# Performance work log

Hardware: AMD Instinct MI355X
Metric: run time of the kernel (lower is better)

The kernel has to match this reference:

```python
import jax, jax.numpy as jnp
import numpy as np

B, S, D, H = 1, 4096, 768, 12
HD = D // H  # 64

def setup_inputs() -> dict:
    key = jax.random.key(0)
    k1, k2, k3 = jax.random.split(key, 3)
    x = jax.random.normal(k1, (B, S, D), dtype=jnp.float32)
    W_attn = jax.random.normal(k2, (D, 3 * D), dtype=jnp.float32) * 0.02
    b_attn = jnp.zeros((3 * D,), dtype=jnp.float32)
    W_proj = jax.random.normal(k3, (D, D), dtype=jnp.float32) * 0.02
    b_proj = jnp.zeros((D,), dtype=jnp.float32)
    return {"x": x, "W_attn": W_attn, "b_attn": b_attn, "W_proj": W_proj, "b_proj": b_proj}

def reference(x, W_attn, b_attn, W_proj, b_proj):
    # qkv projection (Conv1D = x @ W + b)
    qkv = x @ W_attn + b_attn  # [B,S,3D]
    q, k, v = jnp.split(qkv, 3, axis=-1)
    def split_heads(t):
        return t.reshape(B, S, H, HD).transpose(0, 2, 1, 3)  # [B,H,S,HD]
    q, k, v = split_heads(q), split_heads(k), split_heads(v)
    # NOTE: original applies no 1/sqrt(head_dim) scaling
    scores = jnp.einsum('bhqd,bhkd->bhqk', q, k)  # [B,H,S,S]
    causal = jnp.tril(jnp.ones((S, S), dtype=bool))
    mask_value = jnp.finfo(scores.dtype).min
    scores = jnp.where(causal, scores, mask_value)
    attn = jax.nn.softmax(scores, axis=-1)
    # dropout is identity in eval mode
    out = jnp.einsum('bhqk,bhkd->bhqd', attn, v)  # [B,H,S,HD]
    out = out.transpose(0, 2, 1, 3).reshape(B, S, D)
    return out @ W_proj + b_proj
```

## Files before the change

kernel.cpp:

```cpp
#include <hip/hip_runtime.h>


typedef short bf16x8 __attribute__((ext_vector_type(8)));
typedef float f32x4 __attribute__((ext_vector_type(4)));
typedef unsigned short u16x8_t __attribute__((ext_vector_type(8)));
typedef unsigned short u16x4_t __attribute__((ext_vector_type(4)));

#define ATT_S  4096
#define ATT_D  768
#define ATT_3D 2304
#define ATT_H  12
#define LOG2E  1.44269504089f

__device__ __forceinline__ unsigned short f2b(float f) {
  union { float f; unsigned int u; } v; v.f = f;
  unsigned int r = v.u + 0x7fffu + ((v.u >> 16) & 1u);
  return (unsigned short)(r >> 16);
}

__device__ __forceinline__ f32x4 mfma16(bf16x8 a, bf16x8 b, f32x4 c) {
  return __builtin_amdgcn_mfma_f32_16x16x32_bf16(a, b, c, 0, 0, 0);
}

__device__ __forceinline__ void glds16(const void* g, void* l) {
  __builtin_amdgcn_global_load_lds((__attribute__((address_space(1))) void*)g,
                                   (__attribute__((address_space(3))) void*)l,
                                   16, 0, 0);
}

__device__ __forceinline__ int swz8(int row, int c) {
  return row * 64 + ((c ^ (row & 7)) << 3);
}


__global__ __launch_bounds__(256) void convert_f32_bf16(
    const float* __restrict__ in, unsigned short* __restrict__ out, int n4) {
  int i = blockIdx.x * 256 + threadIdx.x;
  if (i >= n4) return;
  float4 v = ((const float4*)in)[i];
  u16x4_t o;
  o[0] = f2b(v.x); o[1] = f2b(v.y); o[2] = f2b(v.z); o[3] = f2b(v.w);
  ((u16x4_t*)out)[i] = o;
}

__global__ __launch_bounds__(256) void transpose_conv(
    const float* __restrict__ W, unsigned short* __restrict__ WT, int K, int N) {
  __shared__ float tile[32][33];
  int bx = blockIdx.x, by = blockIdx.y;
  int tx = threadIdx.x & 31, ty = threadIdx.x >> 5;
#pragma unroll
  for (int k = 0; k < 4; k++)
    tile[ty + k * 8][tx] = W[(size_t)(by * 32 + ty + k * 8) * N + bx * 32 + tx];
  __syncthreads();
#pragma unroll
  for (int k = 0; k < 4; k++)
    WT[(size_t)(bx * 32 + ty + k * 8) * K + by * 32 + tx] = f2b(tile[tx][ty + k * 8]);
}


template <int BF16_OUT>
__global__ __launch_bounds__(256) void gemm_bias(
    const unsigned short* __restrict__ A, const unsigned short* __restrict__ Bt,
    const float* __restrict__ bias, void* __restrict__ Cout,
    int M, int N, int K) {
  __shared__ unsigned short As[128 * 32];
  __shared__ unsigned short Bs[128 * 32];
  const int t = threadIdx.x;
  const int lane = t & 63;
  const int wave = t >> 6;
  const int wr = wave >> 1, wc = wave & 1;
  const int rl = lane & 15, rg = lane >> 4;

  const int nbn = N >> 7;
  const int nwg = gridDim.x;
  const int bid = blockIdx.x;
  const int cpx = nwg >> 3;
  const int swz = (bid & 7) * cpx + (bid >> 3);
  const int bm = swz / nbn, bn = swz % nbn;

  const unsigned short* Ab = A + (size_t)bm * 128 * K;
  const unsigned short* Bb = Bt + (size_t)bn * 128 * K;

  f32x4 acc[4][4];
#pragma unroll
  for (int m = 0; m < 4; m++)
#pragma unroll
    for (int n = 0; n < 4; n++) acc[m][n] = (f32x4){0.f, 0.f, 0.f, 0.f};

  for (int kt = 0; kt < K; kt += 32) {
    if (kt) __syncthreads();
#pragma unroll
    for (int it = 0; it < 2; ++it) {
      int idx = it * 256 + t;
      int row = idx >> 2;
      int slot = idx & 3;
      int sl2 = slot ^ ((row >> 1) & 3);
      unsigned short* ldsA = As + (size_t)(it * 256 + wave * 64) * 8;
      unsigned short* ldsB = Bs + (size_t)(it * 256 + wave * 64) * 8;
      glds16(Ab + (size_t)row * K + kt + sl2 * 8, ldsA);
      glds16(Bb + (size_t)row * K + kt + sl2 * 8, ldsB);
    }
    __syncthreads();

    bf16x8 a[4], b[4];
#pragma unroll
    for (int m = 0; m < 4; m++) {
      int row = wr * 64 + m * 16 + rl;
      int sl2 = rg ^ ((row >> 1) & 3);
      a[m] = *(const bf16x8*)&As[row * 32 + sl2 * 8];
    }
#pragma unroll
    for (int n = 0; n < 4; n++) {
      int row = wc * 64 + n * 16 + rl;
      int sl2 = rg ^ ((row >> 1) & 3);
      b[n] = *(const bf16x8*)&Bs[row * 32 + sl2 * 8];
    }
#pragma unroll
    for (int m = 0; m < 4; m++)
#pragma unroll
      for (int n = 0; n < 4; n++)
        acc[m][n] = mfma16(a[m], b[n], acc[m][n]);
  }

#pragma unroll
  for (int n = 0; n < 4; n++) {
    int col = bn * 128 + wc * 64 + n * 16 + rl;
    float bv = bias[col];
#pragma unroll
    for (int m = 0; m < 4; m++) {
      int row0 = bm * 128 + wr * 64 + m * 16 + rg * 4;
#pragma unroll
      for (int i = 0; i < 4; i++) {
        float v = acc[m][n][i] + bv;
        if (BF16_OUT)
          ((unsigned short*)Cout)[(size_t)(row0 + i) * N + col] = f2b(v);
        else
          ((float*)Cout)[(size_t)(row0 + i) * N + col] = v;
      }
    }
  }
}


__global__ __launch_bounds__(256) void attn_fwd(
    const unsigned short* __restrict__ qkv, unsigned short* __restrict__ aout) {
  __shared__ unsigned short Kb[2][64 * 64];
  __shared__ unsigned short Vb[2][64 * 64];
  __shared__ unsigned short Ps[4][16 * 64];

  const int tid = threadIdx.x;
  const int lane = tid & 63;
  const int w = tid >> 6;
  const int rl = lane & 15, rg = lane >> 4;

  const int bid = blockIdx.x;
  const int h = bid % ATT_H;
  const int qb = 63 - (bid / ATT_H);
  const int qbase = qb * 64 + w * 16;
  const int nt = qb + 1;

  unsigned short* Pw = Ps[w];
  const int skey = lane >> 3;
  const int slot = lane & 7;

  bf16x8 qf[2];
#pragma unroll
  for (int ks = 0; ks < 2; ks++)
    qf[ks] = *(const bf16x8*)&qkv[(size_t)(qbase + rl) * ATT_3D + h * 64 + ks * 32 + rg * 8];

  float mS = -3.0e38f, lS = 0.f;
  f32x4 oacc[4];
#pragma unroll
  for (int hf = 0; hf < 4; hf++) oacc[hf] = (f32x4){0.f, 0.f, 0.f, 0.f};

  u16x8_t kr[2], vr[2];
  const size_t gstep = (size_t)64 * ATT_3D;
  size_t gbase = (size_t)(w * 8 + skey) * ATT_3D + 768 + h * 64 + slot * 8;

#pragma unroll
  for (int it = 0; it < 2; ++it) {
    kr[it] = *(const u16x8_t*)&qkv[gbase + it * 32 * ATT_3D];
    vr[it] = *(const u16x8_t*)&qkv[gbase + it * 32 * ATT_3D + 768];
  }
  {
#pragma unroll
    for (int it = 0; it < 2; ++it) {
      int key = it * 32 + w * 8 + skey;
      *(u16x8_t*)&Kb[0][swz8(key, slot)] = kr[it];
      *(u16x8_t*)&Pw[swz8(it * 8 + skey, slot)] = vr[it];
    }
#pragma unroll
    for (int kk = 0; kk < 2; ++kk) {
      u16x8_t g;
#pragma unroll
      for (int j = 0; j < 8; j++)
        g[j] = Pw[swz8(kk * 8 + j, lane >> 3) + (lane & 7)];
      *(u16x8_t*)&Vb[0][swz8(lane, kk * 4 + w)] = g;
    }
  }
  __syncthreads();

  for (int t = 0; t < nt; ++t) {
    const int cur = t & 1;
    const bool pref = (t + 1 < nt);
    if (pref) {
      size_t gb = gbase + (size_t)(t + 1) * gstep;
#pragma unroll
      for (int it = 0; it < 2; ++it) {
        kr[it] = *(const u16x8_t*)&qkv[gb + it * 32 * ATT_3D];
        vr[it] = *(const u16x8_t*)&qkv[gb + it * 32 * ATT_3D + 768];
      }
    }

    f32x4 st[4];
#pragma unroll
    for (int kf = 0; kf < 4; kf++) st[kf] = (f32x4){0.f, 0.f, 0.f, 0.f};
    __builtin_amdgcn_s_setprio(1);
#pragma unroll
    for (int ks = 0; ks < 2; ks++) {
#pragma unroll
      for (int kf = 0; kf < 4; kf++) {
        bf16x8 kfr = *(const bf16x8*)&Kb[cur][swz8(kf * 16 + rl, ks * 4 + rg)];
        st[kf] = mfma16(kfr, qf[ks], st[kf]);
      }
    }
    __builtin_amdgcn_s_setprio(0);

    if (t == nt - 1) {
#pragma unroll
      for (int kf = 0; kf < 4; kf++)
#pragma unroll
        for (int i = 0; i < 4; i++) {
          int key = t * 64 + kf * 16 + rg * 4 + i;
          if (key > qbase + rl) st[kf][i] = -3.0e38f;
        }
    }

    float pm = st[0][0];
#pragma unroll
    for (int kf = 0; kf < 4; kf++)
#pragma unroll
      for (int i = 0; i < 4; i++) pm = fmaxf(pm, st[kf][i]);
    pm = fmaxf(pm, __shfl_xor(pm, 16, 64));
    pm = fmaxf(pm, __shfl_xor(pm, 32, 64));
    if (!__all(pm - mS <= 8.f)) {
      float mn = fmaxf(mS, pm);
      float fac = __expf(mS - mn);
      mS = mn;
      lS *= fac;
#pragma unroll
      for (int i = 0; i < 4; i++) {
        float fi = __shfl(fac, rg * 4 + i, 64);
#pragma unroll
        for (int hf = 0; hf < 4; hf++) oacc[hf][i] *= fi;
      }
    }
    const float mC = mS * LOG2E;
    float psum = 0.f;
#pragma unroll
    for (int kf = 0; kf < 4; kf++) {
      u16x4_t pw4;
#pragma unroll
      for (int i = 0; i < 4; i++) {
        float p = __builtin_amdgcn_exp2f(fmaf(st[kf][i], LOG2E, -mC));
        psum += p;
        pw4[i] = f2b(p);
      }
      *(u16x4_t*)&Pw[swz8(rl, kf * 2 + (rg >> 1)) + (rg & 1) * 4] = pw4;
    }
    psum += __shfl_xor(psum, 16, 64);
    psum += __shfl_xor(psum, 32, 64);
    lS += psum;

    __builtin_amdgcn_s_setprio(1);
#pragma unroll
    for (int ks2 = 0; ks2 < 2; ks2++) {
      bf16x8 pa = *(const bf16x8*)&Pw[swz8(rl, ks2 * 4 + rg)];
#pragma unroll
      for (int hf = 0; hf < 4; hf++) {
        bf16x8 vbf = *(const bf16x8*)&Vb[cur][swz8(hf * 16 + rl, ks2 * 4 + rg)];
        oacc[hf] = mfma16(pa, vbf, oacc[hf]);
      }
    }
    __builtin_amdgcn_s_setprio(0);

    if (pref) {
      const int nxt = cur ^ 1;
#pragma unroll
      for (int it = 0; it < 2; ++it) {
        int key = it * 32 + w * 8 + skey;
        *(u16x8_t*)&Kb[nxt][swz8(key, slot)] = kr[it];
        *(u16x8_t*)&Pw[swz8(it * 8 + skey, slot)] = vr[it];
      }
#pragma unroll
      for (int kk = 0; kk < 2; ++kk) {
        u16x8_t g;
#pragma unroll
        for (int j = 0; j < 8; j++)
          g[j] = Pw[swz8(kk * 8 + j, lane >> 3) + (lane & 7)];
        *(u16x8_t*)&Vb[nxt][swz8(lane, kk * 4 + w)] = g;
      }
    }
    __syncthreads();
  }

#pragma unroll
  for (int i = 0; i < 4; i++) {
    float li = __shfl(lS, rg * 4 + i, 64);
    float inv = 1.f / li;
    int q = qbase + rg * 4 + i;
#pragma unroll
    for (int hf = 0; hf < 4; hf++)
      aout[(size_t)q * ATT_D + h * 64 + hf * 16 + rl] = f2b(oacc[hf][i] * inv);
  }
}


extern "C" void kernel_launch(void* const* d_in, const int* in_sizes, int n_in,
                              void* d_out, int out_size, void* d_ws, size_t ws_size,
                              hipStream_t stream) {
  const float* x      = (const float*)d_in[0];
  const float* W_attn = (const float*)d_in[1];
  const float* b_attn = (const float*)d_in[2];
  const float* W_proj = (const float*)d_in[3];
  const float* b_proj = (const float*)d_in[4];
  float* out = (float*)d_out;

  char* ws = (char*)d_ws;
  unsigned short* xb  = (unsigned short*)(ws);
  unsigned short* WaT = (unsigned short*)(ws + 6291456);
  unsigned short* WpT = (unsigned short*)(ws + 9830400);
  unsigned short* qkv = (unsigned short*)(ws + 11010048);
  unsigned short* ao  = (unsigned short*)(ws + 29884416);

  convert_f32_bf16<<<3072, 256, 0, stream>>>(x, xb, 786432);
  transpose_conv<<<dim3(72, 24), 256, 0, stream>>>(W_attn, WaT, 768, 2304);
  transpose_conv<<<dim3(24, 24), 256, 0, stream>>>(W_proj, WpT, 768, 768);

  gemm_bias<1><<<576, 256, 0, stream>>>(xb, WaT, b_attn, qkv, 4096, 2304, 768);
  attn_fwd<<<768, 256, 0, stream>>>(qkv, ao);
  gemm_bias<0><<<192, 256, 0, stream>>>(ao, WpT, b_proj, out, 4096, 768, 768);
}
```

Measured before the change: 148.4 us.

## Split long causal attention rows into KV chunks with a combine kernel

Query blocks past the first 16 now have their key range split into chunks of up to 16 tiles, each handled by its own block. Every chunk writes a normalized partial output together with its running max and sum, and a new combine kernel merges the chunks with softmax rescaling. The aim is to balance work across blocks and raise the number of blocks available to fill the GPU, since the causal mask leaves late query blocks with far more key tiles than early ones. In exchange it adds an extra kernel launch, scratch traffic through workspace memory that reuses the x and weight buffers, and extra bf16 rounding of the partial results.

```diff
diff --git a/kernel.cpp b/kernel.cpp
--- a/kernel.cpp
+++ b/kernel.cpp
@@ -16,6 +16,10 @@
   union { float f; unsigned int u; } v; v.f = f;
   unsigned int r = v.u + 0x7fffu + ((v.u >> 16) & 1u);
   return (unsigned short)(r >> 16);
+}
+__device__ __forceinline__ float b2f(unsigned short b) {
+  union { unsigned int u; float f; } v; v.u = ((unsigned int)b) << 16;
+  return v.f;
 }
 
 __device__ __forceinline__ f32x4 mfma16(bf16x8 a, bf16x8 b, f32x4 c) {
@@ -143,7 +147,8 @@
 
 
 __global__ __launch_bounds__(256) void attn_fwd(
-    const unsigned short* __restrict__ qkv, unsigned short* __restrict__ aout) {
+    const unsigned short* __restrict__ qkv, unsigned short* __restrict__ aout,
+    unsigned short* __restrict__ pscr, float* __restrict__ ml) {
   __shared__ unsigned short Kb[2][64 * 64];
   __shared__ unsigned short Vb[2][64 * 64];
   __shared__ unsigned short Ps[4][16 * 64];
@@ -155,9 +160,17 @@
 
   const int bid = blockIdx.x;
   const int h = bid % ATT_H;
-  const int qb = 63 - (bid / ATT_H);
+  const int u = 159 - (bid / ATT_H);
+  int qb, ck;
+  if (u < 16)      { qb = u;                 ck = 0; }
+  else if (u < 48) { qb = 16 + ((u - 16) >> 1); ck = (u - 16) & 1; }
+  else if (u < 96) { qb = 32 + (u - 48) / 3;    ck = (u - 48) % 3; }
+  else             { qb = 48 + ((u - 96) >> 2); ck = (u - 96) & 3; }
+
+  const int nt = qb + 1;
+  const int t0 = ck * 16;
+  const int t1 = min(nt, t0 + 16);
   const int qbase = qb * 64 + w * 16;
-  const int nt = qb + 1;
 
   unsigned short* Pw = Ps[w];
   const int skey = lane >> 3;
@@ -179,8 +192,8 @@
 
 #pragma unroll
   for (int it = 0; it < 2; ++it) {
-    kr[it] = *(const u16x8_t*)&qkv[gbase + it * 32 * ATT_3D];
-    vr[it] = *(const u16x8_t*)&qkv[gbase + it * 32 * ATT_3D + 768];
+    kr[it] = *(const u16x8_t*)&qkv[gbase + (size_t)t0 * gstep + it * 32 * ATT_3D];
+    vr[it] = *(const u16x8_t*)&qkv[gbase + (size_t)t0 * gstep + it * 32 * ATT_3D + 768];
   }
   {
 #pragma unroll
@@ -200,9 +213,9 @@
   }
   __syncthreads();
 
-  for (int t = 0; t < nt; ++t) {
+  for (int t = t0; t < t1; ++t) {
     const int cur = t & 1;
-    const bool pref = (t + 1 < nt);
+    const bool pref = (t + 1 < t1);
     if (pref) {
       size_t gb = gbase + (size_t)(t + 1) * gstep;
 #pragma unroll
@@ -304,15 +317,89 @@
     __syncthreads();
   }
 
+  const bool split = (qb >= 16);
+  unsigned short* dst;
+  int pitch;
+  if (!split || ck == 0) {
+    dst = aout + (size_t)(qb * 64) * ATT_D + h * 64;
+    pitch = ATT_D;
+  } else {
+    int s;
+    if (qb < 32)      s = h * 96 + (qb - 16);
+    else if (qb < 48) s = h * 96 + 16 + (qb - 32) * 2 + (ck - 1);
+    else              s = h * 96 + 48 + (qb - 48) * 3 + (ck - 1);
+    dst = pscr + (size_t)s * 4096;
+    pitch = 64;
+  }
+  if (split && rg == 0) {
+    int unit = h * 48 + (qb - 16);
+    float2* mlp = (float2*)ml;
+    mlp[(unit * 4 + ck) * 64 + w * 16 + rl] = make_float2(mS, lS);
+  }
 #pragma unroll
   for (int i = 0; i < 4; i++) {
     float li = __shfl(lS, rg * 4 + i, 64);
     float inv = 1.f / li;
-    int q = qbase + rg * 4 + i;
+    int qrow = w * 16 + rg * 4 + i;
 #pragma unroll
     for (int hf = 0; hf < 4; hf++)
-      aout[(size_t)q * ATT_D + h * 64 + hf * 16 + rl] = f2b(oacc[hf][i] * inv);
-  }
+      dst[(size_t)qrow * pitch + hf * 16 + rl] = f2b(oacc[hf][i] * inv);
+  }
+}
+
+
+__global__ __launch_bounds__(256) void attn_combine(
+    const unsigned short* __restrict__ pscr, const float* __restrict__ ml,
+    unsigned short* __restrict__ ao) {
+  const int unit = blockIdx.x;
+  const int h = unit / 48, uqb = unit % 48, qb = uqb + 16;
+  const int nch = (qb + 16) >> 4;
+  const int tid = threadIdx.x;
+  const int q = tid >> 2, part = tid & 3;
+
+  const float2* mlp = (const float2*)ml;
+  float m[4], l[4];
+  float M = -3.0e38f;
+  for (int c = 0; c < nch; ++c) {
+    float2 p = mlp[(unit * 4 + c) * 64 + q];
+    m[c] = p.x; l[c] = p.y;
+    M = fmaxf(M, m[c]);
+  }
+  float wgt[4], den = 0.f;
+  for (int c = 0; c < nch; ++c) {
+    wgt[c] = l[c] * __expf(m[c] - M);
+    den += wgt[c];
+  }
+
+  float acc[16];
+#pragma unroll
+  for (int j = 0; j < 16; j++) acc[j] = 0.f;
+
+  unsigned short* aorow = ao + (size_t)(qb * 64 + q) * ATT_D + h * 64 + part * 16;
+  for (int c = 0; c < nch; ++c) {
+    const unsigned short* src;
+    if (c == 0) {
+      src = aorow;
+    } else {
+      int s;
+      if (qb < 32)      s = h * 96 + (qb - 16);
+      else if (qb < 48) s = h * 96 + 16 + (qb - 32) * 2 + (c - 1);
+      else              s = h * 96 + 48 + (qb - 48) * 3 + (c - 1);
+      src = pscr + (size_t)s * 4096 + q * 64 + part * 16;
+    }
+    u16x8_t v0 = *(const u16x8_t*)src;
+    u16x8_t v1 = *(const u16x8_t*)(src + 8);
+#pragma unroll
+    for (int j = 0; j < 8; j++) acc[j] += wgt[c] * b2f(v0[j]);
+#pragma unroll
+    for (int j = 0; j < 8; j++) acc[8 + j] += wgt[c] * b2f(v1[j]);
+  }
+  float inv = 1.f / den;
+  u16x8_t o0, o1;
+#pragma unroll
+  for (int j = 0; j < 8; j++) { o0[j] = f2b(acc[j] * inv); o1[j] = f2b(acc[8 + j] * inv); }
+  *(u16x8_t*)aorow = o0;
+  *(u16x8_t*)(aorow + 8) = o1;
 }
 
 
@@ -332,12 +419,16 @@
   unsigned short* WpT = (unsigned short*)(ws + 9830400);
   unsigned short* qkv = (unsigned short*)(ws + 11010048);
   unsigned short* ao  = (unsigned short*)(ws + 29884416);
+  unsigned short* pscr = (unsigned short*)(ws);
+  float*          ml   = (float*)(ws + 9830400);
 
   convert_f32_bf16<<<3072, 256, 0, stream>>>(x, xb, 786432);
   transpose_conv<<<dim3(72, 24), 256, 0, stream>>>(W_attn, WaT, 768, 2304);
+
+  gemm_bias<1><<<576, 256, 0, stream>>>(xb, WaT, b_attn, qkv, 4096, 2304, 768);
+  attn_fwd<<<1920, 256, 0, stream>>>(qkv, ao, pscr, ml);
+  attn_combine<<<576, 256, 0, stream>>>(pscr, ml, ao);
+
   transpose_conv<<<dim3(24, 24), 256, 0, stream>>>(W_proj, WpT, 768, 768);
-
-  gemm_bias<1><<<576, 256, 0, stream>>>(xb, WaT, b_attn, qkv, 4096, 2304, 768);
-  attn_fwd<<<768, 256, 0, stream>>>(qkv, ao);
   gemm_bias<0><<<192, 256, 0, stream>>>(ao, WpT, b_proj, out, 4096, 768, 768);
 }
```

Result: faster. 129.1 us (-13.0%).
